# Kernel tuning notes

Hardware: AMD Instinct MI355X
Metric: run time of the kernel (lower is better)

The kernel has to match this reference:

```python
import jax, jax.numpy as jnp
import numpy as np

N, IN_DIM, OUT_DIM, NUM_HOPS, SD = 8192, 256, 256, 4, 64
ETA, LAM_LAP, LAM_SP, EPS = 0.5, 0.3, 0.05, 0.5
LN_EPS = 1e-5


def setup_inputs() -> dict:
    key = jax.random.key(0)
    ks = jax.random.split(key, 6)
    K = NUM_HOPS + 1
    return {
        "H": jax.random.normal(ks[0], (N, IN_DIM), jnp.float32),
        "hops": jax.random.normal(ks[1], (K, N, IN_DIM), jnp.float32),
        "L": jax.random.normal(ks[2], (N, N), jnp.float32),
        "U": jax.random.normal(ks[3], (K, IN_DIM, SD), jnp.float32) * 0.1,
        "W_in": jax.random.normal(ks[4], (OUT_DIM, IN_DIM), jnp.float32) * 0.05,
        "ln_gamma": jnp.ones((OUT_DIM,), jnp.float32),
        "ln_beta": jnp.zeros((OUT_DIM,), jnp.float32),
        "log_tau": jnp.zeros((), jnp.float32),
    }


def _per_hop(U_k, H_k):
    n = H_k.shape[0]
    Q, _ = jnp.linalg.qr(U_k)                 # [in_dim, sd]
    Z = Q.T @ H_k.T                           # [sd, n]
    G = Z @ Z.T                               # [sd, sd] Gram, reused
    Sigma = G / (n + 1e-8)
    tr_S = jnp.trace(Sigma)
    tr_S2 = jnp.sum(Sigma * Sigma)            # trace(Sigma @ Sigma), Sigma symmetric
    rank_eff = tr_S ** 2 / (tr_S2 + 1e-8)
    coeff = SD / (n * EPS ** 2 + 1e-8)
    M = jnp.eye(SD, dtype=Z.dtype) + coeff * G
    Lc = jnp.linalg.cholesky(M)
    MiZ = jax.scipy.linalg.cho_solve((Lc, True), Z)  # [sd, n]
    grad_R = (Q @ MiZ).T                      # [n, in_dim]
    return rank_eff, grad_R


def reference(H, hops, L, U, W_in, ln_gamma, ln_beta, log_tau):
    tau = jnp.clip(jnp.exp(log_tau), 0.1, 10.0)
    rank_effs, grads_R = jax.vmap(_per_hop)(U, hops)      # [K], [K,n,in_dim]
    lap_terms = jnp.einsum('nm,kmd->knd', L, hops)        # [K,n,in_dim]
    w = jax.nn.softmax(rank_effs / tau)                   # [K]
    grad_sum = jnp.einsum('k,knd->nd', w, grads_R)
    lap_sum = jnp.einsum('k,knd->nd', w, lap_terms)
    H_half = H + ETA * grad_sum - ETA * LAM_LAP * lap_sum
    H_prox = jnp.sign(H_half) * jax.nn.relu(jnp.abs(H_half) - LAM_SP * ETA)
    H_out = H_prox @ W_in.T
    mu = jnp.mean(H_out, axis=-1, keepdims=True)
    var = jnp.var(H_out, axis=-1, keepdims=True)
    H_out = (H_out - mu) * jax.lax.rsqrt(var + LN_EPS) * ln_gamma + ln_beta
    return H_out, rank_effs, w
```

## Files before the change

kernel.cpp:

```cpp
#include <hip/hip_runtime.h>
#include <stdint.h>


typedef __attribute__((ext_vector_type(8))) short  s16x8;
typedef __attribute__((ext_vector_type(4))) float  f32x4;

#define NNODE 8192
#define DIN   256
#define KHOP  5
#define SDM   64

static const size_t OFF_Q    = 0;
static const size_t OFF_QT   = OFF_Q   + (size_t)5*256*64*4;
static const size_t OFF_ZT   = OFF_QT  + (size_t)5*64*256*2;
static const size_t OFF_GP   = OFF_ZT  + (size_t)5*8192*64*2;
static const size_t OFF_LM   = OFF_GP  + (size_t)5*16*4096*4;
static const size_t OFF_RD   = OFF_LM  + (size_t)5*4096*4;
static const size_t OFF_LU   = OFF_RD  + (size_t)5*64*4;
static const size_t OFF_RDU  = OFF_LU  + (size_t)5*4096*4;
static const size_t OFF_RE   = OFF_RDU + (size_t)5*64*4;
static const size_t OFF_W    = OFF_RE  + 64;
static const size_t OFF_T2   = OFF_W   + 64;
static const size_t OFF_HWT  = OFF_T2  + (size_t)5*256*64*2;
static const size_t OFF_WBF  = OFF_HWT + (size_t)256*8192*2;
static const size_t OFF_HP   = OFF_WBF + (size_t)256*256*2;
static const size_t OFF_PART = OFF_HP  + (size_t)8192*256*2;
static const size_t OFF_LBF  = OFF_PART + (size_t)9*8192*256*2;

__device__ __forceinline__ unsigned short f2bf(float f){
  unsigned u = __builtin_bit_cast(unsigned, f);
  u += 0x7FFFu + ((u >> 16) & 1u);
  return (unsigned short)(u >> 16);
}
__device__ __forceinline__ float bf2f(unsigned h){
  return __builtin_bit_cast(float, h << 16);
}
__device__ __forceinline__ void gl_lds16(const void* g, void* l){
  __builtin_amdgcn_global_load_lds(
      (const __attribute__((address_space(1))) void*)g,
      (__attribute__((address_space(3))) void*)l, 16, 0, 0);
}
__device__ __forceinline__ f32x4 mfma16(s16x8 a, s16x8 b, f32x4 c){
  return __builtin_amdgcn_mfma_f32_16x16x32_bf16(a, b, c, 0, 0, 0);
}

__device__ __forceinline__ void wave_chol64(float* a, float& rdk, int lane){
  rdk = 0.0f;
  #pragma unroll
  for (int j = 0; j < 64; ++j){
    float dj  = __shfl(a[j], j);
    float d   = sqrtf(fmaxf(dj, 1e-20f));
    float rdj = 1.0f / d;
    float cj  = a[j] * rdj;
    a[j] = cj;
    if (lane == j) rdk = rdj;
    #pragma unroll
    for (int l = j+1; l < 64; ++l)
      a[l] -= cj * __shfl(cj, l);
  }
}

__global__ __launch_bounds__(256) void k_pre(const float* __restrict__ U,
                                             const float* __restrict__ L,
                                             float* __restrict__ Lu,
                                             float* __restrict__ rdu,
                                             unsigned short* __restrict__ Lbf){
  __shared__ float A[64*65];
  int tid = threadIdx.x;
  if (blockIdx.x >= 5){
    size_t base = (size_t)(blockIdx.x - 5);
    #pragma unroll 4
    for (int it = 0; it < 16; ++it){
      size_t e = ((base + (size_t)it*2048)*256 + tid)*8;
      f32x4 a = *(const f32x4*)(L + e);
      f32x4 b = *(const f32x4*)(L + e + 4);
      uint4 u;
      u.x = (unsigned)f2bf(a[0]) | ((unsigned)f2bf(a[1]) << 16);
      u.y = (unsigned)f2bf(a[2]) | ((unsigned)f2bf(a[3]) << 16);
      u.z = (unsigned)f2bf(b[0]) | ((unsigned)f2bf(b[1]) << 16);
      u.w = (unsigned)f2bf(b[2]) | ((unsigned)f2bf(b[3]) << 16);
      *(uint4*)(Lbf + e) = u;
    }
    return;
  }
  int k = blockIdx.x;
  const float* Uk = U + (size_t)k*16384;
  int ti = tid >> 4, tj = tid & 15;
  float s[16];
  #pragma unroll
  for (int i = 0; i < 16; ++i) s[i] = 0.0f;
  for (int n = 0; n < 256; ++n){
    f32x4 xa = *(const f32x4*)(Uk + n*64 + ti*4);
    f32x4 xb = *(const f32x4*)(Uk + n*64 + tj*4);
    #pragma unroll
    for (int p = 0; p < 4; ++p)
      #pragma unroll
      for (int q = 0; q < 4; ++q) s[p*4+q] += xa[p]*xb[q];
  }
  #pragma unroll
  for (int p = 0; p < 4; ++p)
    #pragma unroll
    for (int q = 0; q < 4; ++q) A[(ti*4+p)*65 + tj*4+q] = s[p*4+q];
  __syncthreads();
  if (tid < 64){
    int lane = tid;
    float a[64];
    #pragma unroll
    for (int l = 0; l < 64; ++l) a[l] = A[lane*65 + l];
    float rdk;
    wave_chol64(a, rdk, lane);
    #pragma unroll
    for (int l = 0; l < 64; ++l) Lu[(size_t)k*4096 + lane*64 + l] = a[l];
    rdu[k*64 + lane] = rdk;
  }
}

__global__ __launch_bounds__(256) void k_qsolve(const float* __restrict__ U,
                                                const float* __restrict__ Lu,
                                                const float* __restrict__ rdu,
                                                float* __restrict__ Qf,
                                                unsigned short* __restrict__ Qt){
  int k = blockIdx.y, tid = threadIdx.x, wave = tid >> 6, lane = tid & 63;
  __shared__ float Al[64*65];
  __shared__ float rds[64];
  for (int e = tid; e < 4096; e += 256) Al[(e>>6)*65 + (e&63)] = Lu[(size_t)k*4096 + e];
  if (tid < 64) rds[tid] = rdu[k*64 + tid];
  __syncthreads();
  int n = blockIdx.x*4 + wave;
  float x = U[((size_t)k*256 + n)*64 + lane];
  #pragma unroll
  for (int j = 0; j < 64; ++j){
    float zj = __shfl(x, j) * rds[j];
    x = (lane == j) ? zj : (lane > j ? x - Al[lane*65+j]*zj : x);
  }
  Qf[((size_t)k*256 + n)*64 + lane] = x;
  Qt[(size_t)k*16384 + lane*256 + n] = f2bf(x);
}

__global__ __launch_bounds__(256,2) void k_zgemm(const float* __restrict__ hops,
                                                 const unsigned short* __restrict__ Qt,
                                                 unsigned short* __restrict__ Zt){
  __shared__ __align__(16) unsigned short Al[128][72];
  __shared__ __align__(16) unsigned short Bl[64][64];
  int tid = threadIdx.x, lane = tid & 63, wave = tid >> 6;
  int q = lane >> 4, r = lane & 15;
  int k = blockIdx.y, m0 = blockIdx.x * 128;
  f32x4 acc[2][4];
  #pragma unroll
  for (int a = 0; a < 2; ++a)
    #pragma unroll
    for (int b = 0; b < 4; ++b) acc[a][b] = (f32x4){0,0,0,0};
  int rr = tid >> 1, half = tid & 1;
  for (int it = 0; it < 4; ++it){
    __syncthreads();
    #pragma unroll
    for (int i = 0; i < 2; ++i){
      int o = i*4096 + wave*1024 + lane*16;
      int srow = o >> 7, kc = (o & 127) >> 1;
      gl_lds16(Qt + (size_t)k*16384 + srow*256 + it*64 + kc,
               (char*)&Bl[0][0] + i*4096 + wave*1024);
    }
    const float* ga = hops + ((size_t)k*NNODE + m0 + rr)*256 + it*64 + half*32;
    f32x4 v[8];
    #pragma unroll
    for (int i = 0; i < 8; ++i) v[i] = *(const f32x4*)(ga + i*4);
    #pragma unroll
    for (int i = 0; i < 4; ++i){
      s16x8 t;
      #pragma unroll
      for (int j = 0; j < 8; ++j){ int e = i*8+j; t[j] = (short)f2bf(v[e>>2][e&3]); }
      *(s16x8*)&Al[rr][half*32 + i*8] = t;
    }
    __syncthreads();
    #pragma unroll
    for (int h = 0; h < 2; ++h){
      int ko = h*32 + q*8;
      s16x8 b[4];
      #pragma unroll
      for (int ni = 0; ni < 4; ++ni) b[ni] = *(const s16x8*)&Bl[ni*16 + r][ko];
      #pragma unroll
      for (int mi = 0; mi < 2; ++mi){
        s16x8 a = *(const s16x8*)&Al[wave*32 + mi*16 + r][ko];
        #pragma unroll
        for (int ni = 0; ni < 4; ++ni) acc[mi][ni] = mfma16(a, b[ni], acc[mi][ni]);
      }
    }
  }
  #pragma unroll
  for (int mi = 0; mi < 2; ++mi)
    #pragma unroll
    for (int ni = 0; ni < 4; ++ni)
      #pragma unroll
      for (int ii = 0; ii < 4; ++ii){
        int m = m0 + wave*32 + mi*16 + q*4 + ii;
        int sc = ni*16 + r;
        Zt[((size_t)k*NNODE + m)*64 + sc] = f2bf(acc[mi][ni][ii]);
      }
}

__global__ __launch_bounds__(256) void k_gpart(const unsigned short* __restrict__ Zt,
                                               float* __restrict__ Gp){
  int k = blockIdx.x, c = blockIdx.y, tid = threadIdx.x;
  __shared__ __align__(16) unsigned short Zl[128][64];
  int ti = tid >> 4, tj = tid & 15;
  float acc[16];
  #pragma unroll
  for (int i = 0; i < 16; ++i) acc[i] = 0.0f;
  for (int sub = 0; sub < 4; ++sub){
    const char* gb = (const char*)Zt + ((size_t)k*NNODE + c*512 + sub*128)*128;
    __syncthreads();
    #pragma unroll
    for (int i = 0; i < 4; ++i){
      int o = i*4096 + tid*16;
      *(uint4*)((char*)&Zl[0][0] + o) = *(const uint4*)(gb + o);
    }
    __syncthreads();
    for (int n = 0; n < 128; ++n){
      const unsigned short* row = &Zl[n][0];
      uint2 ua = *(const uint2*)(row + ti*4);
      uint2 ub = *(const uint2*)(row + tj*4);
      float xa[4] = { bf2f(ua.x & 0xffff), bf2f(ua.x >> 16), bf2f(ua.y & 0xffff), bf2f(ua.y >> 16) };
      float xb[4] = { bf2f(ub.x & 0xffff), bf2f(ub.x >> 16), bf2f(ub.y & 0xffff), bf2f(ub.y >> 16) };
      #pragma unroll
      for (int p = 0; p < 4; ++p)
        #pragma unroll
        for (int qn = 0; qn < 4; ++qn) acc[p*4+qn] += xa[p]*xb[qn];
    }
  }
  float* o = Gp + ((size_t)k*16 + c)*4096;
  #pragma unroll
  for (int p = 0; p < 4; ++p)
    #pragma unroll
    for (int qn = 0; qn < 4; ++qn) o[(ti*4+p)*64 + tj*4+qn] = acc[p*4+qn];
}

__global__ __launch_bounds__(256) void k_gred(const float* __restrict__ Gp,
                                              float* __restrict__ LmO,
                                              float* __restrict__ rdO,
                                              float* __restrict__ reO){
  int k = blockIdx.x, tid = threadIdx.x;
  __shared__ float A[64*65];
  __shared__ float red[256];
  int ti = tid >> 4, tj = tid & 15;
  float s[16];
  #pragma unroll
  for (int i = 0; i < 16; ++i) s[i] = 0.0f;
  for (int c = 0; c < 16; ++c){
    const float* g = Gp + ((size_t)k*16 + c)*4096 + (ti*4)*64 + tj*4;
    #pragma unroll
    for (int p = 0; p < 4; ++p)
      #pragma unroll
      for (int qn = 0; qn < 4; ++qn) s[p*4+qn] += g[p*64+qn];
  }
  const float sc    = 1.0f / (8192.0f + 1e-8f);
  const float coeff = 64.0f / (8192.0f*0.25f + 1e-8f);
  float trp = 0.0f, tr2p = 0.0f;
  #pragma unroll
  for (int p = 0; p < 4; ++p)
    #pragma unroll
    for (int qn = 0; qn < 4; ++qn){
      float gg = s[p*4+qn];
      float sg = gg * sc;
      tr2p += sg*sg;
      int row = ti*4+p, col = tj*4+qn;
      if (row == col) trp += sg;
      A[row*65 + col] = (row == col ? 1.0f : 0.0f) + coeff*gg;
    }
  red[tid] = trp; __syncthreads();
  for (int o = 128; o > 0; o >>= 1){ if (tid < o) red[tid] += red[tid+o]; __syncthreads(); }
  float tr = red[0]; __syncthreads();
  red[tid] = tr2p; __syncthreads();
  for (int o = 128; o > 0; o >>= 1){ if (tid < o) red[tid] += red[tid+o]; __syncthreads(); }
  float tr2 = red[0];
  if (tid == 0) reO[k] = tr*tr / (tr2 + 1e-8f);
  __syncthreads();
  if (tid < 64){
    int lane = tid;
    float a[64];
    #pragma unroll
    for (int l = 0; l < 64; ++l) a[l] = A[lane*65 + l];
    float rdk;
    wave_chol64(a, rdk, lane);
    #pragma unroll
    for (int l = 0; l < 64; ++l) LmO[(size_t)k*4096 + lane*64 + l] = a[l];
    rdO[k*64 + lane] = rdk;
  }
}

__global__ void k_soft(const float* __restrict__ re, const float* __restrict__ ltau,
                       float* __restrict__ wv, float* __restrict__ dtail){
  if (threadIdx.x == 0){
    float tau = expf(ltau[0]);
    tau = fminf(fmaxf(tau, 0.1f), 10.0f);
    float r[5], m = -1e30f;
    for (int i = 0; i < 5; ++i){ r[i] = re[i]; m = fmaxf(m, r[i]); }
    float e[5], sum = 0.0f;
    for (int i = 0; i < 5; ++i){ e[i] = expf((r[i]-m)/tau); sum += e[i]; }
    for (int i = 0; i < 5; ++i){
      float w = e[i]/sum;
      wv[i] = w; dtail[i] = r[i]; dtail[5+i] = w;
    }
  }
}

__global__ __launch_bounds__(256) void k_post(const float* __restrict__ hops,
                                              const float* __restrict__ wv,
                                              unsigned short* __restrict__ hwT,
                                              const float* __restrict__ Qf,
                                              const float* __restrict__ LmI,
                                              const float* __restrict__ rdI,
                                              unsigned short* __restrict__ T2w,
                                              const float* __restrict__ Win,
                                              unsigned short* __restrict__ Wbf){
  __shared__ float T[64*65];
  __shared__ float rds[64];
  int bid = blockIdx.x, tid = threadIdx.x;
  if (bid < 512){
    int n0 = (bid & 127)*64, d0 = (bid >> 7)*64;
    float wl[5];
    #pragma unroll
    for (int k = 0; k < 5; ++k) wl[k] = -0.15f * wv[k];
    for (int e = tid; e < 1024; e += 256){
      int row = e >> 4, c4 = (e & 15)*4;
      f32x4 acc = (f32x4){0,0,0,0};
      #pragma unroll
      for (int k = 0; k < 5; ++k){
        f32x4 v = *(const f32x4*)(hops + ((size_t)k*NNODE + n0 + row)*256 + d0 + c4);
        acc += v * wl[k];
      }
      T[row*65 + c4+0] = acc[0]; T[row*65 + c4+1] = acc[1];
      T[row*65 + c4+2] = acc[2]; T[row*65 + c4+3] = acc[3];
    }
    __syncthreads();
    for (int e = tid; e < 1024; e += 256){
      int dr = e >> 4, c4 = (e & 15)*4;
      unsigned short h0 = f2bf(T[(c4+0)*65 + dr]);
      unsigned short h1 = f2bf(T[(c4+1)*65 + dr]);
      unsigned short h2 = f2bf(T[(c4+2)*65 + dr]);
      unsigned short h3 = f2bf(T[(c4+3)*65 + dr]);
      uint2 u; u.x = (unsigned)h0 | ((unsigned)h1 << 16); u.y = (unsigned)h2 | ((unsigned)h3 << 16);
      *(uint2*)(hwT + (size_t)(d0+dr)*NNODE + n0 + c4) = u;
    }
  } else if (bid < 832){
    int i = bid - 512;
    int k = i >> 6, xb = i & 63;
    int wave = tid >> 6, lane = tid & 63;
    for (int e = tid; e < 4096; e += 256) T[(e>>6)*65 + (e&63)] = LmI[(size_t)k*4096 + e];
    if (tid < 64) rds[tid] = rdI[k*64 + tid];
    __syncthreads();
    int n = xb*4 + wave;
    float x = Qf[((size_t)k*256 + n)*64 + lane];
    #pragma unroll
    for (int j = 0; j < 64; ++j){
      float zj = __shfl(x, j) * rds[j];
      x = (lane == j) ? zj : (lane > j ? x - T[lane*65+j]*zj : x);
    }
    #pragma unroll
    for (int j = 63; j >= 0; --j){
      float yj = __shfl(x, j) * rds[j];
      x = (lane == j) ? yj : (lane < j ? x - T[j*65+lane]*yj : x);
    }
    float scale = 0.5f * wv[k];
    T2w[((size_t)k*256 + n)*64 + lane] = f2bf(scale * x);
  } else {
    int i = bid - 832;
    int e = (i*256 + tid)*4;
    f32x4 v = *(const f32x4*)(Win + e);
    uint2 u;
    u.x = (unsigned)f2bf(v[0]) | ((unsigned)f2bf(v[1]) << 16);
    u.y = (unsigned)f2bf(v[2]) | ((unsigned)f2bf(v[3]) << 16);
    *(uint2*)(Wbf + e) = u;
  }
}

__global__ __launch_bounds__(256,2) void k_gg(const unsigned short* __restrict__ Lbf,
                                              const unsigned short* __restrict__ Bt,
                                              unsigned short* __restrict__ part,
                                              const unsigned short* __restrict__ Zt,
                                              const unsigned short* __restrict__ T2w){
  __shared__ __align__(16) unsigned short SM[24960];
  int bid = blockIdx.x, tid = threadIdx.x;
  int lane = tid & 63, wave = tid >> 6;
  int q = lane >> 4, r = lane & 15;
  if (bid < 512){
    unsigned short* Al = SM;
    unsigned short* Bl = SM + 16*520;
    int m0 = (bid & 63) * 128;
    int by = bid >> 6;
    size_t kbase = (size_t)by * 1024;
    int sr = lane >> 3, sc8 = (lane & 7) * 8;
    f32x4 acc[8][4];
    #pragma unroll
    for (int a = 0; a < 8; ++a)
      #pragma unroll
      for (int b = 0; b < 4; ++b) acc[a][b] = (f32x4){0,0,0,0};
    for (int it = 0; it < 16; ++it){
      size_t k0 = kbase + it*64;
      __syncthreads();
      #pragma unroll
      for (int i = 0; i < 12; ++i){
        int c = i*4 + wave;
        if (c < 16){
          gl_lds16(Lbf + (size_t)(m0 + c*8 + sr)*NNODE + k0 + sc8,
                   (char*)Al + c*1040 + lane*16);
        } else {
          int cb = c - 16;
          gl_lds16(Bt + (size_t)(cb*8 + sr)*NNODE + k0 + sc8,
                   (char*)Bl + cb*1040 + lane*16);
        }
      }
      __syncthreads();
      #pragma unroll
      for (int h = 0; h < 2; ++h){
        int ko = h*32 + q*8;
        s16x8 b[4];
        #pragma unroll
        for (int ni = 0; ni < 4; ++ni){
          int d = wave*64 + ni*16 + r;
          b[ni] = *(const s16x8*)(Bl + (d>>3)*520 + (d&7)*64 + ko);
        }
        #pragma unroll
        for (int mi = 0; mi < 8; ++mi){
          int m = mi*16 + r;
          s16x8 a = *(const s16x8*)(Al + (m>>3)*520 + (m&7)*64 + ko);
          #pragma unroll
          for (int ni = 0; ni < 4; ++ni) acc[mi][ni] = mfma16(a, b[ni], acc[mi][ni]);
        }
      }
    }
    unsigned short* o = part + (size_t)by * 2097152;
    #pragma unroll
    for (int mi = 0; mi < 8; ++mi)
      #pragma unroll
      for (int ni = 0; ni < 4; ++ni)
        #pragma unroll
        for (int ii = 0; ii < 4; ++ii){
          int m = m0 + mi*16 + q*4 + ii;
          int n = wave*64 + ni*16 + r;
          o[(size_t)m*256 + n] = f2bf(acc[mi][ni][ii]);
        }
  } else {
    unsigned short* Al = SM;
    unsigned short* Bl = SM + 2048;
    int m0 = (bid - 512) * 32;
    f32x4 acc[2][4];
    #pragma unroll
    for (int a = 0; a < 2; ++a)
      #pragma unroll
      for (int b = 0; b < 4; ++b) acc[a][b] = (f32x4){0,0,0,0};
    for (int kk = 0; kk < 5; ++kk){
      __syncthreads();
      {
        int o = wave*1024 + lane*16;
        gl_lds16((const char*)Zt + ((size_t)kk*NNODE + m0)*128 + o,
                 (char*)Al + wave*1024);
      }
      #pragma unroll
      for (int i = 0; i < 8; ++i){
        int o = i*4096 + wave*1024 + lane*16;
        gl_lds16((const char*)T2w + (size_t)kk*32768 + o,
                 (char*)Bl + i*4096 + wave*1024);
      }
      __syncthreads();
      #pragma unroll
      for (int h = 0; h < 2; ++h){
        int ko = h*32 + q*8;
        s16x8 b[4];
        #pragma unroll
        for (int ni = 0; ni < 4; ++ni) b[ni] = *(const s16x8*)&Bl[(wave*64 + ni*16 + r)*64 + ko];
        #pragma unroll
        for (int mi = 0; mi < 2; ++mi){
          s16x8 a = *(const s16x8*)&Al[(mi*16 + r)*64 + ko];
          #pragma unroll
          for (int ni = 0; ni < 4; ++ni) acc[mi][ni] = mfma16(a, b[ni], acc[mi][ni]);
        }
      }
    }
    unsigned short* o8 = part + (size_t)8 * 2097152;
    #pragma unroll
    for (int mi = 0; mi < 2; ++mi)
      #pragma unroll
      for (int ni = 0; ni < 4; ++ni)
        #pragma unroll
        for (int ii = 0; ii < 4; ++ii){
          int m = m0 + mi*16 + q*4 + ii;
          int n = wave*64 + ni*16 + r;
          o8[(size_t)m*256 + n] = f2bf(acc[mi][ni][ii]);
        }
  }
}

__global__ __launch_bounds__(256) void k_combine(const float* __restrict__ H,
                                                 const unsigned short* __restrict__ part,
                                                 unsigned short* __restrict__ Hp){
  size_t e = ((size_t)blockIdx.x*256 + threadIdx.x)*4;
  f32x4 h = *(const f32x4*)(H + e);
  float s0 = h[0], s1 = h[1], s2 = h[2], s3 = h[3];
  #pragma unroll
  for (int sl = 0; sl < 9; ++sl){
    uint2 u = *(const uint2*)(part + (size_t)sl*2097152 + e);
    s0 += bf2f(u.x & 0xffff); s1 += bf2f(u.x >> 16);
    s2 += bf2f(u.y & 0xffff); s3 += bf2f(u.y >> 16);
  }
  #define PROX(a) ({ float _t = fabsf(a) - 0.025f; _t > 0.0f ? copysignf(_t,(a)) : 0.0f; })
  uint2 o;
  o.x = (unsigned)f2bf(PROX(s0)) | ((unsigned)f2bf(PROX(s1)) << 16);
  o.y = (unsigned)f2bf(PROX(s2)) | ((unsigned)f2bf(PROX(s3)) << 16);
  *(uint2*)(Hp + e) = o;
}

__global__ __launch_bounds__(256,2) void k_finln(const unsigned short* __restrict__ Hp,
                                                 const unsigned short* __restrict__ Wbf,
                                                 const float* __restrict__ gamma,
                                                 const float* __restrict__ beta,
                                                 float* __restrict__ out){
  __shared__ __align__(16) unsigned short Al[64][64];
  __shared__ __align__(16) unsigned short Bl[256][64];
  __shared__ float SmR[64][4];
  __shared__ float SqR[64][4];
  int tid = threadIdx.x, lane = tid & 63, wave = tid >> 6;
  int q = lane >> 4, r = lane & 15;
  int m0 = blockIdx.x * 64;
  f32x4 acc[4][4];
  #pragma unroll
  for (int a = 0; a < 4; ++a)
    #pragma unroll
    for (int b = 0; b < 4; ++b) acc[a][b] = (f32x4){0,0,0,0};
  for (int it = 0; it < 4; ++it){
    __syncthreads();
    #pragma unroll
    for (int i = 0; i < 2; ++i){
      int o = i*4096 + wave*1024 + lane*16;
      int row = o >> 7, kc = o & 127;
      gl_lds16((const char*)Hp + (size_t)(m0+row)*512 + it*128 + kc,
               (char*)&Al[0][0] + i*4096 + wave*1024);
    }
    #pragma unroll
    for (int i = 0; i < 8; ++i){
      int o = i*4096 + wave*1024 + lane*16;
      int n = o >> 7, kc = o & 127;
      gl_lds16((const char*)Wbf + (size_t)n*512 + it*128 + kc,
               (char*)&Bl[0][0] + i*4096 + wave*1024);
    }
    __syncthreads();
    #pragma unroll
    for (int h = 0; h < 2; ++h){
      int ko = h*32 + q*8;
      s16x8 b[4];
      #pragma unroll
      for (int ni = 0; ni < 4; ++ni) b[ni] = *(const s16x8*)&Bl[wave*64 + ni*16 + r][ko];
      #pragma unroll
      for (int mi = 0; mi < 4; ++mi){
        s16x8 a = *(const s16x8*)&Al[mi*16 + r][ko];
        #pragma unroll
        for (int ni = 0; ni < 4; ++ni) acc[mi][ni] = mfma16(a, b[ni], acc[mi][ni]);
      }
    }
  }
  #pragma unroll
  for (int mi = 0; mi < 4; ++mi)
    #pragma unroll
    for (int ii = 0; ii < 4; ++ii){
      float sm = 0.0f, sq = 0.0f;
      #pragma unroll
      for (int ni = 0; ni < 4; ++ni){
        float v = acc[mi][ni][ii];
        sm += v; sq += v*v;
      }
      #pragma unroll
      for (int o = 1; o < 16; o <<= 1){ sm += __shfl_xor(sm, o, 64); sq += __shfl_xor(sq, o, 64); }
      if (r == 0){
        int rl = mi*16 + q*4 + ii;
        SmR[rl][wave] = sm; SqR[rl][wave] = sq;
      }
    }
  __syncthreads();
  float g[4], b[4];
  #pragma unroll
  for (int ni = 0; ni < 4; ++ni){
    g[ni] = gamma[wave*64 + ni*16 + r];
    b[ni] = beta [wave*64 + ni*16 + r];
  }
  #pragma unroll
  for (int mi = 0; mi < 4; ++mi)
    #pragma unroll
    for (int ii = 0; ii < 4; ++ii){
      int rl = mi*16 + q*4 + ii;
      float sm = SmR[rl][0] + SmR[rl][1] + SmR[rl][2] + SmR[rl][3];
      float sq = SqR[rl][0] + SqR[rl][1] + SqR[rl][2] + SqR[rl][3];
      float mean = sm * (1.0f/256.0f);
      float var  = sq * (1.0f/256.0f) - mean*mean;
      float rs   = rsqrtf(var + 1e-5f);
      #pragma unroll
      for (int ni = 0; ni < 4; ++ni){
        out[(size_t)(m0+rl)*256 + wave*64 + ni*16 + r] =
            (acc[mi][ni][ii] - mean)*rs*g[ni] + b[ni];
      }
    }
}

extern "C" void kernel_launch(void* const* d_in, const int* in_sizes, int n_in,
                              void* d_out, int out_size, void* d_ws, size_t ws_size,
                              hipStream_t stream){
  const float* H    = (const float*)d_in[0];
  const float* hops = (const float*)d_in[1];
  const float* Lmat = (const float*)d_in[2];
  const float* U    = (const float*)d_in[3];
  const float* Win  = (const float*)d_in[4];
  const float* gam  = (const float*)d_in[5];
  const float* bet  = (const float*)d_in[6];
  const float* ltau = (const float*)d_in[7];
  float* out = (float*)d_out;

  char* ws = (char*)d_ws;
  float*          Qf   = (float*)(ws + OFF_Q);
  unsigned short* Qt   = (unsigned short*)(ws + OFF_QT);
  unsigned short* Zt   = (unsigned short*)(ws + OFF_ZT);
  float*          Gp   = (float*)(ws + OFF_GP);
  float*          Lm   = (float*)(ws + OFF_LM);
  float*          rdw  = (float*)(ws + OFF_RD);
  float*          Lu   = (float*)(ws + OFF_LU);
  float*          rdu  = (float*)(ws + OFF_RDU);
  float*          re   = (float*)(ws + OFF_RE);
  float*          wv   = (float*)(ws + OFF_W);
  unsigned short* T2w  = (unsigned short*)(ws + OFF_T2);
  unsigned short* hwT  = (unsigned short*)(ws + OFF_HWT);
  unsigned short* Wbf  = (unsigned short*)(ws + OFF_WBF);
  unsigned short* Hp   = (unsigned short*)(ws + OFF_HP);
  unsigned short* part = (unsigned short*)(ws + OFF_PART);
  unsigned short* Lbf  = (unsigned short*)(ws + OFF_LBF);

  hipLaunchKernelGGL(k_pre,    dim3(2053),   dim3(256), 0, stream, U, Lmat, Lu, rdu, Lbf);
  hipLaunchKernelGGL(k_qsolve, dim3(64,5),   dim3(256), 0, stream, U, Lu, rdu, Qf, Qt);
  hipLaunchKernelGGL(k_zgemm,  dim3(64,5),   dim3(256), 0, stream, hops, Qt, Zt);
  hipLaunchKernelGGL(k_gpart,  dim3(5,16),   dim3(256), 0, stream, Zt, Gp);
  hipLaunchKernelGGL(k_gred,   dim3(5),      dim3(256), 0, stream, Gp, Lm, rdw, re);
  hipLaunchKernelGGL(k_soft,   dim3(1),      dim3(64),  0, stream, re, ltau, wv, out + 2097152);
  hipLaunchKernelGGL(k_post,   dim3(896),    dim3(256), 0, stream, hops, wv, hwT, Qf, Lm, rdw, T2w, Win, Wbf);
  hipLaunchKernelGGL(k_gg,     dim3(768),    dim3(256), 0, stream, Lbf, hwT, part, Zt, T2w);
  hipLaunchKernelGGL(k_combine,dim3(2048),   dim3(256), 0, stream, H, part, Hp);
  hipLaunchKernelGGL(k_finln,  dim3(128),    dim3(256), 0, stream, Hp, Wbf, gam, bet, out);
}
```

Before: 628.1 us.

## Fuse L bf16 conversion into GEMM A-load with register prefetch; fuse combine into final LN

Removes the separate pass that converts the 8192x8192 fp32 L matrix to bf16. The big GEMM now reads fp32 L directly, converts it in registers, and writes it to LDS, prefetching the next K-tile into registers during the MFMA loop. The combine/prox kernel is also folded into the final projection+LayerNorm kernel, so the Hp round trip and one launch go away. The cost is more register pressure in k_gg and fp32 (double-width) global reads of L inside the GEMM. With only 128 blocks, the finln kernel now also does all of the reduction of the 9 partial slices.

```diff
diff --git a/kernel.cpp b/kernel.cpp
--- a/kernel.cpp
+++ b/kernel.cpp
@@ -25,7 +25,6 @@
 static const size_t OFF_WBF  = OFF_HWT + (size_t)256*8192*2;
 static const size_t OFF_HP   = OFF_WBF + (size_t)256*256*2;
 static const size_t OFF_PART = OFF_HP  + (size_t)8192*256*2;
-static const size_t OFF_LBF  = OFF_PART + (size_t)9*8192*256*2;
 
 __device__ __forceinline__ unsigned short f2bf(float f){
   unsigned u = __builtin_bit_cast(unsigned, f);
@@ -61,28 +60,10 @@
 }
 
 __global__ __launch_bounds__(256) void k_pre(const float* __restrict__ U,
-                                             const float* __restrict__ L,
                                              float* __restrict__ Lu,
-                                             float* __restrict__ rdu,
-                                             unsigned short* __restrict__ Lbf){
+                                             float* __restrict__ rdu){
   __shared__ float A[64*65];
   int tid = threadIdx.x;
-  if (blockIdx.x >= 5){
-    size_t base = (size_t)(blockIdx.x - 5);
-    #pragma unroll 4
-    for (int it = 0; it < 16; ++it){
-      size_t e = ((base + (size_t)it*2048)*256 + tid)*8;
-      f32x4 a = *(const f32x4*)(L + e);
-      f32x4 b = *(const f32x4*)(L + e + 4);
-      uint4 u;
-      u.x = (unsigned)f2bf(a[0]) | ((unsigned)f2bf(a[1]) << 16);
-      u.y = (unsigned)f2bf(a[2]) | ((unsigned)f2bf(a[3]) << 16);
-      u.z = (unsigned)f2bf(b[0]) | ((unsigned)f2bf(b[1]) << 16);
-      u.w = (unsigned)f2bf(b[2]) | ((unsigned)f2bf(b[3]) << 16);
-      *(uint4*)(Lbf + e) = u;
-    }
-    return;
-  }
   int k = blockIdx.x;
   const float* Uk = U + (size_t)k*16384;
   int ti = tid >> 4, tj = tid & 15;
@@ -373,7 +354,7 @@
   }
 }
 
-__global__ __launch_bounds__(256,2) void k_gg(const unsigned short* __restrict__ Lbf,
+__global__ __launch_bounds__(256,2) void k_gg(const float* __restrict__ Lf,
                                               const unsigned short* __restrict__ Bt,
                                               unsigned short* __restrict__ part,
                                               const unsigned short* __restrict__ Zt,
@@ -389,27 +370,37 @@
     int by = bid >> 6;
     size_t kbase = (size_t)by * 1024;
     int sr = lane >> 3, sc8 = (lane & 7) * 8;
+    int ar = tid >> 1, ah = tid & 1;
+    unsigned short* adst = Al + (ar>>3)*520 + (ar&7)*64 + ah*32;
+    const float* abase = Lf + (size_t)(m0 + ar)*NNODE + ah*32;
     f32x4 acc[8][4];
     #pragma unroll
     for (int a = 0; a < 8; ++a)
       #pragma unroll
       for (int b = 0; b < 4; ++b) acc[a][b] = (f32x4){0,0,0,0};
+    f32x4 av[8];
+    #pragma unroll
+    for (int j = 0; j < 8; ++j) av[j] = *(const f32x4*)(abase + kbase + j*4);
+    #pragma unroll
+    for (int i = 0; i < 8; ++i){
+      int cb = i*4 + wave;
+      gl_lds16(Bt + (size_t)(cb*8 + sr)*NNODE + kbase + sc8,
+               (char*)Bl + cb*1040 + lane*16);
+    }
+    #pragma unroll
+    for (int j = 0; j < 4; ++j){
+      s16x8 t;
+      #pragma unroll
+      for (int e = 0; e < 8; ++e) t[e] = (short)f2bf(av[j*2 + (e>>2)][e&3]);
+      *(s16x8*)(adst + j*8) = t;
+    }
+    __syncthreads();
     for (int it = 0; it < 16; ++it){
-      size_t k0 = kbase + it*64;
-      __syncthreads();
-      #pragma unroll
-      for (int i = 0; i < 12; ++i){
-        int c = i*4 + wave;
-        if (c < 16){
-          gl_lds16(Lbf + (size_t)(m0 + c*8 + sr)*NNODE + k0 + sc8,
-                   (char*)Al + c*1040 + lane*16);
-        } else {
-          int cb = c - 16;
-          gl_lds16(Bt + (size_t)(cb*8 + sr)*NNODE + k0 + sc8,
-                   (char*)Bl + cb*1040 + lane*16);
-        }
-      }
-      __syncthreads();
+      size_t k1 = kbase + (it+1)*64;
+      if (it < 15){
+        #pragma unroll
+        for (int j = 0; j < 8; ++j) av[j] = *(const f32x4*)(abase + k1 + j*4);
+      }
       #pragma unroll
       for (int h = 0; h < 2; ++h){
         int ko = h*32 + q*8;
@@ -427,6 +418,23 @@
           for (int ni = 0; ni < 4; ++ni) acc[mi][ni] = mfma16(a, b[ni], acc[mi][ni]);
         }
       }
+      __syncthreads();
+      if (it < 15){
+        #pragma unroll
+        for (int i = 0; i < 8; ++i){
+          int cb = i*4 + wave;
+          gl_lds16(Bt + (size_t)(cb*8 + sr)*NNODE + k1 + sc8,
+                   (char*)Bl + cb*1040 + lane*16);
+        }
+        #pragma unroll
+        for (int j = 0; j < 4; ++j){
+          s16x8 t;
+          #pragma unroll
+          for (int e = 0; e < 8; ++e) t[e] = (short)f2bf(av[j*2 + (e>>2)][e&3]);
+          *(s16x8*)(adst + j*8) = t;
+        }
+      }
+      __syncthreads();
     }
     unsigned short* o = part + (size_t)by * 2097152;
     #pragma unroll
@@ -490,37 +498,36 @@
   }
 }
 
-__global__ __launch_bounds__(256) void k_combine(const float* __restrict__ H,
+__global__ __launch_bounds__(256,2) void k_finln(const float* __restrict__ H,
                                                  const unsigned short* __restrict__ part,
-                                                 unsigned short* __restrict__ Hp){
-  size_t e = ((size_t)blockIdx.x*256 + threadIdx.x)*4;
-  f32x4 h = *(const f32x4*)(H + e);
-  float s0 = h[0], s1 = h[1], s2 = h[2], s3 = h[3];
-  #pragma unroll
-  for (int sl = 0; sl < 9; ++sl){
-    uint2 u = *(const uint2*)(part + (size_t)sl*2097152 + e);
-    s0 += bf2f(u.x & 0xffff); s1 += bf2f(u.x >> 16);
-    s2 += bf2f(u.y & 0xffff); s3 += bf2f(u.y >> 16);
-  }
-  #define PROX(a) ({ float _t = fabsf(a) - 0.025f; _t > 0.0f ? copysignf(_t,(a)) : 0.0f; })
-  uint2 o;
-  o.x = (unsigned)f2bf(PROX(s0)) | ((unsigned)f2bf(PROX(s1)) << 16);
-  o.y = (unsigned)f2bf(PROX(s2)) | ((unsigned)f2bf(PROX(s3)) << 16);
-  *(uint2*)(Hp + e) = o;
-}
-
-__global__ __launch_bounds__(256,2) void k_finln(const unsigned short* __restrict__ Hp,
                                                  const unsigned short* __restrict__ Wbf,
                                                  const float* __restrict__ gamma,
                                                  const float* __restrict__ beta,
                                                  float* __restrict__ out){
-  __shared__ __align__(16) unsigned short Al[64][64];
+  __shared__ __align__(16) unsigned short Hl[64][264];
   __shared__ __align__(16) unsigned short Bl[256][64];
   __shared__ float SmR[64][4];
   __shared__ float SqR[64][4];
   int tid = threadIdx.x, lane = tid & 63, wave = tid >> 6;
   int q = lane >> 4, r = lane & 15;
   int m0 = blockIdx.x * 64;
+  #define PROX(a) ({ float _t = fabsf(a) - 0.025f; _t > 0.0f ? copysignf(_t,(a)) : 0.0f; })
+  for (int g = tid; g < 4096; g += 256){
+    int row = g >> 6, c4 = (g & 63) * 4;
+    size_t e = (size_t)(m0 + row)*256 + c4;
+    f32x4 h = *(const f32x4*)(H + e);
+    float s0 = h[0], s1 = h[1], s2 = h[2], s3 = h[3];
+    #pragma unroll
+    for (int sl = 0; sl < 9; ++sl){
+      uint2 u = *(const uint2*)(part + (size_t)sl*2097152 + e);
+      s0 += bf2f(u.x & 0xffff); s1 += bf2f(u.x >> 16);
+      s2 += bf2f(u.y & 0xffff); s3 += bf2f(u.y >> 16);
+    }
+    uint2 o;
+    o.x = (unsigned)f2bf(PROX(s0)) | ((unsigned)f2bf(PROX(s1)) << 16);
+    o.y = (unsigned)f2bf(PROX(s2)) | ((unsigned)f2bf(PROX(s3)) << 16);
+    *(uint2*)&Hl[row][c4] = o;
+  }
   f32x4 acc[4][4];
   #pragma unroll
   for (int a = 0; a < 4; ++a)
@@ -528,13 +535,6 @@
     for (int b = 0; b < 4; ++b) acc[a][b] = (f32x4){0,0,0,0};
   for (int it = 0; it < 4; ++it){
     __syncthreads();
-    #pragma unroll
-    for (int i = 0; i < 2; ++i){
-      int o = i*4096 + wave*1024 + lane*16;
-      int row = o >> 7, kc = o & 127;
-      gl_lds16((const char*)Hp + (size_t)(m0+row)*512 + it*128 + kc,
-               (char*)&Al[0][0] + i*4096 + wave*1024);
-    }
     #pragma unroll
     for (int i = 0; i < 8; ++i){
       int o = i*4096 + wave*1024 + lane*16;
@@ -545,13 +545,13 @@
     __syncthreads();
     #pragma unroll
     for (int h = 0; h < 2; ++h){
-      int ko = h*32 + q*8;
+      int ko = it*64 + h*32 + q*8;
       s16x8 b[4];
       #pragma unroll
-      for (int ni = 0; ni < 4; ++ni) b[ni] = *(const s16x8*)&Bl[wave*64 + ni*16 + r][ko];
+      for (int ni = 0; ni < 4; ++ni) b[ni] = *(const s16x8*)&Bl[wave*64 + ni*16 + r][h*32 + q*8];
       #pragma unroll
       for (int mi = 0; mi < 4; ++mi){
-        s16x8 a = *(const s16x8*)&Al[mi*16 + r][ko];
+        s16x8 a = *(const s16x8*)&Hl[mi*16 + r][ko];
         #pragma unroll
         for (int ni = 0; ni < 4; ++ni) acc[mi][ni] = mfma16(a, b[ni], acc[mi][ni]);
       }
@@ -626,18 +626,15 @@
   unsigned short* T2w  = (unsigned short*)(ws + OFF_T2);
   unsigned short* hwT  = (unsigned short*)(ws + OFF_HWT);
   unsigned short* Wbf  = (unsigned short*)(ws + OFF_WBF);
-  unsigned short* Hp   = (unsigned short*)(ws + OFF_HP);
   unsigned short* part = (unsigned short*)(ws + OFF_PART);
-  unsigned short* Lbf  = (unsigned short*)(ws + OFF_LBF);
-
-  hipLaunchKernelGGL(k_pre,    dim3(2053),   dim3(256), 0, stream, U, Lmat, Lu, rdu, Lbf);
+
+  hipLaunchKernelGGL(k_pre,    dim3(5),      dim3(256), 0, stream, U, Lu, rdu);
   hipLaunchKernelGGL(k_qsolve, dim3(64,5),   dim3(256), 0, stream, U, Lu, rdu, Qf, Qt);
   hipLaunchKernelGGL(k_zgemm,  dim3(64,5),   dim3(256), 0, stream, hops, Qt, Zt);
   hipLaunchKernelGGL(k_gpart,  dim3(5,16),   dim3(256), 0, stream, Zt, Gp);
   hipLaunchKernelGGL(k_gred,   dim3(5),      dim3(256), 0, stream, Gp, Lm, rdw, re);
   hipLaunchKernelGGL(k_soft,   dim3(1),      dim3(64),  0, stream, re, ltau, wv, out + 2097152);
   hipLaunchKernelGGL(k_post,   dim3(896),    dim3(256), 0, stream, hops, wv, hwT, Qf, Lm, rdw, T2w, Win, Wbf);
-  hipLaunchKernelGGL(k_gg,     dim3(768),    dim3(256), 0, stream, Lbf, hwT, part, Zt, T2w);
-  hipLaunchKernelGGL(k_combine,dim3(2048),   dim3(256), 0, stream, H, part, Hp);
-  hipLaunchKernelGGL(k_finln,  dim3(128),    dim3(256), 0, stream, Hp, Wbf, gam, bet, out);
-}
+  hipLaunchKernelGGL(k_gg,     dim3(768),    dim3(256), 0, stream, Lmat, hwT, part, Zt, T2w);
+  hipLaunchKernelGGL(k_finln,  dim3(128),    dim3(256), 0, stream, H, part, Wbf, gam, bet, out);
+}
```

New measurement: 657.0 us. +4.6%, slower.
